# Kernel optimization log

Hardware: AMD Instinct MI355X
Metric: run time of the kernel (lower is better)

## Reference

```python
import jax, jax.numpy as jnp
import numpy as np

P = 30000    # pathway graph nodes
E = 480000   # edges
G = 20000    # genes
MP = 32      # max pathways per gene (padded)
R = 28       # pathway root count
B = 4096     # batch of gene pairs
IN, H, OUT = 394, 256, 64
GD = 128     # params.gene_dim


def setup_inputs() -> dict:
    key = jax.random.key(0)
    ks = iter(jax.random.split(key, 48))
    nx = lambda shape, s=1.0: jax.random.normal(next(ks), shape, dtype=jnp.float32) * s
    inp = {}
    inp["x1"] = nx((P, IN))
    inp["x2"] = nx((P, IN))
    inp["edge_src"] = jax.random.randint(next(ks), (E,), 0, P)
    inp["edge_dst"] = jax.random.randint(next(ks), (E,), 0, P)
    inp["edge_weight"] = jax.random.uniform(next(ks), (E,), dtype=jnp.float32)
    for g in ("g1", "g2"):
        inp[g + "_w1"] = nx((IN, H), 0.05); inp[g + "_b1"] = jnp.zeros((H,), jnp.float32)
        inp[g + "_w2"] = nx((H, OUT), 0.05); inp[g + "_b2"] = jnp.zeros((OUT,), jnp.float32)
    inp["pl1_w"] = nx((OUT * R, 256), 0.02); inp["pl1_b"] = jnp.zeros((256,), jnp.float32)
    inp["bn1_g"] = jnp.ones((256,), jnp.float32); inp["bn1_b"] = jnp.zeros((256,), jnp.float32)
    inp["pl2_w"] = nx((256, GD), 0.05); inp["pl2_b"] = jnp.zeros((GD,), jnp.float32)
    inp["bn2_g"] = jnp.ones((GD,), jnp.float32); inp["bn2_b"] = jnp.zeros((GD,), jnp.float32)
    inp["fc_w"] = nx((2 * GD, 256), 0.05); inp["fc_b"] = jnp.zeros((256,), jnp.float32)
    inp["fc1_w"] = nx((256, 128), 0.05); inp["fc1_b"] = jnp.zeros((128,), jnp.float32)
    inp["fc2_w"] = nx((128, 1), 0.05); inp["fc2_b"] = jnp.zeros((1,), jnp.float32)
    inp["pathway_root"] = jax.random.randint(next(ks), (P,), 0, R)
    inp["gene_paths"] = jax.random.randint(next(ks), (G, MP), 0, P)
    inp["gene_paths_mask"] = jax.random.uniform(next(ks), (G, MP)) < 0.7
    inp["head_ids"] = jax.random.randint(next(ks), (B,), 0, G)
    inp["tail_ids"] = jax.random.randint(next(ks), (B,), 0, G)
    return inp


def gcn_conv(x, w, b, src, dst, ew):
    # PyG GCNConv with edge weights + self loops (fill_value=1), symmetric norm.
    h = x @ w
    deg = jnp.zeros((x.shape[0],), x.dtype).at[dst].add(ew) + 1.0
    norm = jax.lax.rsqrt(deg)
    msg = h[src] * (ew * norm[src] * norm[dst])[:, None]
    agg = jnp.zeros_like(h).at[dst].add(msg) + h * (norm * norm)[:, None]
    return agg + b


def pathway_gcn(x, w1, b1, w2, b2, src, dst, ew):
    h = jax.nn.relu(gcn_conv(x, w1, b1, src, dst, ew))  # F.dropout in eval = identity
    return gcn_conv(h, w2, b2, src, dst, ew)


def gene_pathway_feat(s, gene_ids, gene_paths, gene_paths_mask, pathway_root):
    # Vectorized form of the per-gene python-loop gather + per-root sum.
    paths = gene_paths[gene_ids]                      # [B, MP]
    m = gene_paths_mask[gene_ids].astype(s.dtype)     # [B, MP]
    gathered = s[paths]                               # [B, MP, 64]
    oh = jax.nn.one_hot(pathway_root[paths], R, dtype=s.dtype) * m[..., None]
    feat = jnp.einsum('bpr,bpd->brd', oh, gathered)   # segment-sum into roots
    return feat.reshape(paths.shape[0], R * s.shape[1])


def batchnorm(x, g, b, eps=1e-5):
    mu = x.mean(0)
    var = x.var(0)  # biased, as torch BN training
    return g * (x - mu) * jax.lax.rsqrt(var + eps) + b


def reference(x1, x2, edge_src, edge_dst, edge_weight,
              g1_w1, g1_b1, g1_w2, g1_b2, g2_w1, g2_b1, g2_w2, g2_b2,
              pl1_w, pl1_b, bn1_g, bn1_b, pl2_w, pl2_b, bn2_g, bn2_b,
              fc_w, fc_b, fc1_w, fc1_b, fc2_w, fc2_b,
              pathway_root, gene_paths, gene_paths_mask, head_ids, tail_ids):
    out1 = pathway_gcn(x1, g1_w1, g1_b1, g1_w2, g1_b2, edge_src, edge_dst, edge_weight)
    out2 = pathway_gcn(x2, g2_w1, g2_b1, g2_w2, g2_b2, edge_src, edge_dst, edge_weight)
    s = out1 + out2  # original stacks feats from both graphs per pathway, then sums

    def fuse(ids):
        f = gene_pathway_feat(s, ids, gene_paths, gene_paths_mask, pathway_root)
        h = jax.nn.relu(batchnorm(f @ pl1_w + pl1_b, bn1_g, bn1_b))
        return batchnorm(h @ pl2_w + pl2_b, bn2_g, bn2_b)

    fuse_feat = jnp.concatenate([fuse(head_ids), fuse(tail_ids)], axis=1)  # [B, 2*GD]
    final = jax.nn.relu(fuse_feat @ fc_w + fc_b) @ fc1_w + fc1_b
    return jax.nn.relu(final) @ fc2_w + fc2_b  # [B, 1]
```

## Files before the change

kernel.cpp:

```cpp
#include <hip/hip_runtime.h>
#include <cstdint>

typedef __attribute__((ext_vector_type(4))) float f32x4;
typedef __attribute__((ext_vector_type(8))) short s16x8;

__device__ inline unsigned short f2bf(float f) {
    unsigned u = __float_as_uint(f);
    unsigned r = (u + 0x7FFFu + ((u >> 16) & 1u)) >> 16;
    return (unsigned short)r;
}
__device__ inline float b2f(unsigned short h) {
    return __uint_as_float(((unsigned)h) << 16);
}

__device__ inline void gload16(const unsigned short* g, unsigned short* l) {
    __builtin_amdgcn_global_load_lds(
        (const __attribute__((address_space(1))) unsigned int*)g,
        (__attribute__((address_space(3))) unsigned int*)l, 16, 0, 0);
}

struct TD { const float* in; unsigned short* out; int K, N, Kp, ldo; };

__global__ void prep_kernel(const unsigned char* __restrict__ mask, int maskBytes,
                            int* __restrict__ flag, float* __restrict__ zspan, long long zwords,
                            TD d0, TD d1, TD d2, TD d3, TD d4, TD d5, TD d6, TD d7) {
    int y = blockIdx.y;
    if (y == 0) {
        if (blockIdx.x != 0) return;
        __shared__ int isByte, isFloat;
        if (threadIdx.x == 0) { isByte = 0; isFloat = 0; }
        __syncthreads();
        const unsigned* w = (const unsigned*)mask;
        for (int i = threadIdx.x; i < maskBytes / 4; i += blockDim.x) {
            unsigned v = w[i];
            if (v == 0u || v == 1u) continue;
            if (v == 0x3f800000u) isFloat = 1; else isByte = 1;
        }
        __syncthreads();
        if (threadIdx.x == 0) *flag = isFloat ? 2 : (isByte ? 1 : 0);
        return;
    }
    if (y == 1) {
        long long i = (long long)blockIdx.x * 256 + threadIdx.x;
        if (i < zwords) zspan[i] = 0.f;
        return;
    }
    TD d = d0;
    if (y == 3) d = d1; else if (y == 4) d = d2; else if (y == 5) d = d3;
    else if (y == 6) d = d4; else if (y == 7) d = d5; else if (y == 8) d = d6; else if (y == 9) d = d7;
    int idx = blockIdx.x * 256 + threadIdx.x;
    if (idx >= d.N * d.Kp) return;
    int n = idx / d.Kp, k = idx - n * d.Kp;
    d.out[(size_t)n * d.ldo + k] = (k < d.K) ? f2bf(d.in[(size_t)k * d.N + n]) : (unsigned short)0;
}

__global__ void deg_cnt_kernel(const int* __restrict__ dst, const float* __restrict__ ew,
                               float* __restrict__ degw, int* __restrict__ cnt, int E) {
    int e = blockIdx.x * 256 + threadIdx.x;
    if (e >= E) return;
    int d = dst[e];
    unsafeAtomicAdd(&degw[d], ew[e]);
    atomicAdd(&cnt[d], 1);
}

__global__ __launch_bounds__(1024) void norm_scan_kernel(const int* __restrict__ cnt,
                                                         int* __restrict__ rowstart,
                                                         float* __restrict__ degw, int P) {
    int t = threadIdx.x;
    if (blockIdx.x > 0) {
        int i = (blockIdx.x - 1) * 1024 + t;
        if (i < P) degw[i] = rsqrtf(degw[i] + 1.0f);
        return;
    }
    const int seg = (P + 1023) >> 10;
    int base = t * seg;
    int sum = 0;
    for (int j = 0; j < seg; ++j) {
        int i = base + j;
        if (i < P) sum += cnt[i];
    }
    int lane = t & 63, w = t >> 6;
    int x = sum;
#pragma unroll
    for (int off = 1; off < 64; off <<= 1) {
        int y = __shfl_up(x, off);
        if (lane >= off) x += y;
    }
    __shared__ int wsum[16];
    if (lane == 63) wsum[w] = x;
    __syncthreads();
    int woff = 0;
    for (int i = 0; i < w; ++i) woff += wsum[i];
    int run = woff + x - sum;
    for (int j = 0; j < seg; ++j) {
        int i = base + j;
        if (i < P) { run += cnt[i]; rowstart[i + 1] = run; }
    }
    if (t == 0) rowstart[0] = 0;
}

__global__ void fill_kernel(const int* __restrict__ src, const int* __restrict__ dst,
                            const float* __restrict__ ew, const float* __restrict__ norm,
                            const int* __restrict__ rowstart, int* __restrict__ fill,
                            int* __restrict__ csrc, float* __restrict__ coef, int E) {
    int e = blockIdx.x * 256 + threadIdx.x;
    if (e >= E) return;
    int d = dst[e], sI = src[e];
    int pos = rowstart[d] + atomicAdd(&fill[d], 1);
    csrc[pos] = sI;
    coef[pos] = ew[e] * norm[sI] * norm[d];
}

__global__ __launch_bounds__(256) void conv1_agg_kernel(
    const unsigned short* __restrict__ Hb, const float* __restrict__ norm,
    const int* __restrict__ rowstart, const int* __restrict__ csrc, const float* __restrict__ coef,
    const float* __restrict__ b0, const float* __restrict__ b1,
    unsigned short* __restrict__ out, int P) {
    int node = blockIdx.x * 4 + (threadIdx.x >> 6);
    if (node >= P) return;
    int z = blockIdx.y;
    const unsigned short* H = Hb + (size_t)z * P * 256;
    const float* bias = z ? b1 : b0;
    int lane = threadIdx.x & 63;
    int f4 = lane * 4;
    float nn = norm[node];
    ushort4 hv = *(const ushort4*)(H + (size_t)node * 256 + f4);
    float a0 = b2f(hv.x) * nn * nn, a1 = b2f(hv.y) * nn * nn;
    float a2 = b2f(hv.z) * nn * nn, a3 = b2f(hv.w) * nn * nn;
    int s0 = rowstart[node], s1 = rowstart[node + 1];
    int p = s0;
    for (; p + 4 <= s1; p += 4) {
        int i0 = csrc[p], i1 = csrc[p + 1], i2 = csrc[p + 2], i3 = csrc[p + 3];
        float c0 = coef[p], c1 = coef[p + 1], c2 = coef[p + 2], c3 = coef[p + 3];
        ushort4 v0 = *(const ushort4*)(H + (size_t)i0 * 256 + f4);
        ushort4 v1 = *(const ushort4*)(H + (size_t)i1 * 256 + f4);
        ushort4 v2 = *(const ushort4*)(H + (size_t)i2 * 256 + f4);
        ushort4 v3 = *(const ushort4*)(H + (size_t)i3 * 256 + f4);
        a0 += b2f(v0.x) * c0 + b2f(v1.x) * c1 + b2f(v2.x) * c2 + b2f(v3.x) * c3;
        a1 += b2f(v0.y) * c0 + b2f(v1.y) * c1 + b2f(v2.y) * c2 + b2f(v3.y) * c3;
        a2 += b2f(v0.z) * c0 + b2f(v1.z) * c1 + b2f(v2.z) * c2 + b2f(v3.z) * c3;
        a3 += b2f(v0.w) * c0 + b2f(v1.w) * c1 + b2f(v2.w) * c2 + b2f(v3.w) * c3;
    }
    for (; p < s1; ++p) {
        int i0 = csrc[p];
        float c0 = coef[p];
        ushort4 v0 = *(const ushort4*)(H + (size_t)i0 * 256 + f4);
        a0 += b2f(v0.x) * c0; a1 += b2f(v0.y) * c0; a2 += b2f(v0.z) * c0; a3 += b2f(v0.w) * c0;
    }
    float4 bv = *(const float4*)(bias + f4);
    ushort4 o;
    o.x = f2bf(fmaxf(a0 + bv.x, 0.f));
    o.y = f2bf(fmaxf(a1 + bv.y, 0.f));
    o.z = f2bf(fmaxf(a2 + bv.z, 0.f));
    o.w = f2bf(fmaxf(a3 + bv.w, 0.f));
    *(ushort4*)(out + (size_t)node * 512 + z * 256 + f4) = o;
}

__global__ __launch_bounds__(256) void conv2_agg_kernel(
    const unsigned short* __restrict__ T, const float* __restrict__ norm,
    const int* __restrict__ rowstart, const int* __restrict__ csrc, const float* __restrict__ coef,
    const float* __restrict__ b0, const float* __restrict__ b1,
    float* __restrict__ s, int P) {
    int node = blockIdx.x * 4 + (threadIdx.x >> 6);
    if (node >= P) return;
    int lane = threadIdx.x & 63;
    float nn = norm[node];
    float acc = b2f(T[(size_t)node * 64 + lane]) * nn * nn;
    int s0 = rowstart[node], s1 = rowstart[node + 1];
    int p = s0;
    for (; p + 4 <= s1; p += 4) {
        int i0 = csrc[p], i1 = csrc[p + 1], i2 = csrc[p + 2], i3 = csrc[p + 3];
        float c0 = coef[p], c1 = coef[p + 1], c2 = coef[p + 2], c3 = coef[p + 3];
        acc += b2f(T[(size_t)i0 * 64 + lane]) * c0 + b2f(T[(size_t)i1 * 64 + lane]) * c1 +
               b2f(T[(size_t)i2 * 64 + lane]) * c2 + b2f(T[(size_t)i3 * 64 + lane]) * c3;
    }
    for (; p < s1; ++p) acc += b2f(T[(size_t)csrc[p] * 64 + lane]) * coef[p];
    s[(size_t)node * 64 + lane] = acc + b0[lane] + b1[lane];
}

struct G2 {
    const void* A[2]; const unsigned short* Bt[2]; const float* bias[2];
    float* Cf[2]; unsigned short* Cb[2];
};

template<int BM, int BN, int WM, int WN>
__global__ __launch_bounds__(256) void gemm1_hybrid_kernel(
    const float* __restrict__ x0, const float* __restrict__ x1,
    const unsigned short* __restrict__ Bt0, const unsigned short* __restrict__ Bt1,
    unsigned short* __restrict__ C0, unsigned short* __restrict__ C1,
    int M, int IN, int Kp, int ldc) {
    const int z = blockIdx.z;
    const float* A = z ? x1 : x0;
    const unsigned short* Bt = z ? Bt1 : Bt0;
    unsigned short* Cb = z ? C1 : C0;

    constexpr int LDK = 40;
    __shared__ __align__(16) unsigned short As[2][BM * LDK];
    __shared__ __align__(16) unsigned short Bs[2][BN * 32];
    const int t = threadIdx.x, lane = t & 63, wid = t >> 6;
    constexpr int NWC = BN / WN;
    const int wr = wid / NWC, wc = wid % NWC;
    constexpr int MR = WM / 16, NR = WN / 16;
    static_assert((BM / WM) * (BN / WN) == 4, "4 waves");
    constexpr int BI = BN / 64;
    const int row0 = blockIdx.y * BM, col0 = blockIdx.x * BN;
    const int sr = lane >> 2;
    const int sc = ((lane & 3) ^ ((lane >> 3) & 3)) * 8;
    int brow[BI];
#pragma unroll
    for (int i = 0; i < BI; ++i) brow[i] = col0 + (wid * BI + i) * 16 + sr;
    const int ar = t >> 2, akc = (t & 3) * 8;
    int arowg = row0 + ar; if (arowg >= M) arowg = M - 1;
    const float* aptr = A + (size_t)arowg * IN;

    f32x4 acc[MR][NR] = {};
    const int r16 = lane & 15, q = lane >> 4;
    const int kbA = q * 8;
    const int kbB = ((q ^ ((r16 >> 1) & 3)) * 8);

    auto stageB = [&](int buf, int kt) {
#pragma unroll
        for (int i = 0; i < BI; ++i)
            gload16(Bt + (size_t)brow[i] * Kp + kt + sc, &Bs[buf][(wid * BI + i) * 512]);
    };
    auto loadA = [&](int kt, float* v) {
        int kg = kt + akc;
        if (kg + 8 <= IN) {
            float2 a = *(const float2*)(aptr + kg);
            float2 b = *(const float2*)(aptr + kg + 2);
            float2 c = *(const float2*)(aptr + kg + 4);
            float2 d = *(const float2*)(aptr + kg + 6);
            v[0]=a.x; v[1]=a.y; v[2]=b.x; v[3]=b.y; v[4]=c.x; v[5]=c.y; v[6]=d.x; v[7]=d.y;
        } else {
#pragma unroll
            for (int j = 0; j < 8; ++j) v[j] = (kg + j < IN) ? aptr[kg + j] : 0.f;
        }
    };
    auto writeA = [&](int buf, const float* v) {
        s16x8 w;
#pragma unroll
        for (int j = 0; j < 8; ++j) w[j] = (short)f2bf(v[j]);
        *(s16x8*)&As[buf][ar * LDK + akc] = w;
    };

    {
        float v[8];
        stageB(0, 0);
        loadA(0, v);
        writeA(0, v);
    }
    int cur = 0;
    for (int kt = 0; kt < Kp; kt += 32) {
        __syncthreads();
        float nv[8];
        const bool has = (kt + 32 < Kp);
        if (has) { stageB(cur ^ 1, kt + 32); loadA(kt + 32, nv); }
        s16x8 af[MR], bfr[NR];
#pragma unroll
        for (int m = 0; m < MR; ++m)
            af[m] = *(const s16x8*)&As[cur][(wr * WM + m * 16 + r16) * LDK + kbA];
#pragma unroll
        for (int n = 0; n < NR; ++n)
            bfr[n] = *(const s16x8*)&Bs[cur][(wc * WN + n * 16 + r16) * 32 + kbB];
#pragma unroll
        for (int m = 0; m < MR; ++m)
#pragma unroll
            for (int n = 0; n < NR; ++n)
                acc[m][n] = __builtin_amdgcn_mfma_f32_16x16x32_bf16(af[m], bfr[n], acc[m][n], 0, 0, 0);
        if (has) writeA(cur ^ 1, nv);
        cur ^= 1;
    }
#pragma unroll
    for (int m = 0; m < MR; ++m)
#pragma unroll
        for (int n = 0; n < NR; ++n) {
            int col = col0 + wc * WN + n * 16 + r16;
#pragma unroll
            for (int r = 0; r < 4; ++r) {
                int row = row0 + wr * WM + m * 16 + q * 4 + r;
                if (row < M) Cb[(size_t)row * ldc + col] = f2bf(acc[m][n][r]);
            }
        }
}

template<int BM, int BN, int WM, int WN>
__global__ __launch_bounds__(256) void m97s_gemm_kernel(
    G2 g, int M, int Kp, int lda, int ldc, int relu) {
    const int z = blockIdx.z;
    const unsigned short* A = (const unsigned short*)(z ? g.A[1] : g.A[0]);
    const unsigned short* Bt = z ? g.Bt[1] : g.Bt[0];
    const float* bias = z ? g.bias[1] : g.bias[0];
    float* Cf = z ? g.Cf[1] : g.Cf[0];
    unsigned short* Cb = z ? g.Cb[1] : g.Cb[0];

    __shared__ __align__(16) unsigned short As[2][BM * 32];
    __shared__ __align__(16) unsigned short Bs[2][BN * 32];
    const int t = threadIdx.x, lane = t & 63, wid = t >> 6;
    constexpr int NWC = BN / WN;
    const int wr = wid / NWC, wc = wid % NWC;
    constexpr int MR = WM / 16, NR = WN / 16;
    static_assert((BM / WM) * (BN / WN) == 4, "4 waves");
    constexpr int AI = BM / 64, BI = BN / 64;
    const int row0 = blockIdx.y * BM, col0 = blockIdx.x * BN;
    const int sr = lane >> 2;
    const int sc = ((lane & 3) ^ ((lane >> 3) & 3)) * 8;
    int arow[AI];
#pragma unroll
    for (int i = 0; i < AI; ++i) {
        int r = row0 + (wid * AI + i) * 16 + sr;
        arow[i] = r < M ? r : M - 1;
    }
    int brow[BI];
#pragma unroll
    for (int i = 0; i < BI; ++i) brow[i] = col0 + (wid * BI + i) * 16 + sr;

    f32x4 acc[MR][NR] = {};
    const int r16 = lane & 15;
    const int kb = (((lane >> 4) ^ ((r16 >> 1) & 3)) * 8);

    auto stage = [&](int buf, int kt) {
#pragma unroll
        for (int i = 0; i < AI; ++i)
            gload16(A + (size_t)arow[i] * lda + kt + sc, &As[buf][(wid * AI + i) * 512]);
#pragma unroll
        for (int i = 0; i < BI; ++i)
            gload16(Bt + (size_t)brow[i] * Kp + kt + sc, &Bs[buf][(wid * BI + i) * 512]);
    };

    stage(0, 0);
    int cur = 0;
    for (int kt = 0; kt < Kp; kt += 32) {
        __syncthreads();
        if (kt + 32 < Kp) stage(cur ^ 1, kt + 32);
        s16x8 af[MR], bfr[NR];
#pragma unroll
        for (int m = 0; m < MR; ++m)
            af[m] = *(const s16x8*)&As[cur][(wr * WM + m * 16 + r16) * 32 + kb];
#pragma unroll
        for (int n = 0; n < NR; ++n)
            bfr[n] = *(const s16x8*)&Bs[cur][(wc * WN + n * 16 + r16) * 32 + kb];
#pragma unroll
        for (int m = 0; m < MR; ++m)
#pragma unroll
            for (int n = 0; n < NR; ++n)
                acc[m][n] = __builtin_amdgcn_mfma_f32_16x16x32_bf16(af[m], bfr[n], acc[m][n], 0, 0, 0);
        cur ^= 1;
    }
#pragma unroll
    for (int m = 0; m < MR; ++m)
#pragma unroll
        for (int n = 0; n < NR; ++n) {
            int col = col0 + wc * WN + n * 16 + r16;
#pragma unroll
            for (int r = 0; r < 4; ++r) {
                int row = row0 + wr * WM + m * 16 + (lane >> 4) * 4 + r;
                if (row < M) {
                    float v = acc[m][n][r] + (bias ? bias[col] : 0.f);
                    if (relu) v = fmaxf(v, 0.f);
                    if (Cf) Cf[(size_t)row * ldc + col] = v;
                    if (Cb) Cb[(size_t)row * ldc + col] = f2bf(v);
                }
            }
        }
}

template<int BM, int BN, int WM, int WN>
__global__ __launch_bounds__(256) void pl1_stats_kernel(
    G2 g, int M, int Kp, int lda, int ldc, float* __restrict__ statsPart, int C) {
    const int z = blockIdx.z;
    const unsigned short* A = (const unsigned short*)(z ? g.A[1] : g.A[0]);
    const unsigned short* Bt = z ? g.Bt[1] : g.Bt[0];
    const float* bias = z ? g.bias[1] : g.bias[0];
    float* Cf = z ? g.Cf[1] : g.Cf[0];

    __shared__ __align__(16) unsigned short As[2][BM * 32];
    __shared__ __align__(16) unsigned short Bs[2][BN * 32];
    const int t = threadIdx.x, lane = t & 63, wid = t >> 6;
    constexpr int NWC = BN / WN;
    const int wr = wid / NWC, wc = wid % NWC;
    constexpr int MR = WM / 16, NR = WN / 16;
    constexpr int AI = BM / 64, BI = BN / 64;
    const int row0 = blockIdx.y * BM, col0 = blockIdx.x * BN;
    const int sr = lane >> 2;
    const int sc = ((lane & 3) ^ ((lane >> 3) & 3)) * 8;
    int arow[AI];
#pragma unroll
    for (int i = 0; i < AI; ++i) {
        int r = row0 + (wid * AI + i) * 16 + sr;
        arow[i] = r < M ? r : M - 1;
    }
    int brow[BI];
#pragma unroll
    for (int i = 0; i < BI; ++i) brow[i] = col0 + (wid * BI + i) * 16 + sr;

    f32x4 acc[MR][NR] = {};
    const int r16 = lane & 15, q = lane >> 4;
    const int kb = ((q ^ ((r16 >> 1) & 3)) * 8);

    auto stage = [&](int buf, int kt) {
#pragma unroll
        for (int i = 0; i < AI; ++i)
            gload16(A + (size_t)arow[i] * lda + kt + sc, &As[buf][(wid * AI + i) * 512]);
#pragma unroll
        for (int i = 0; i < BI; ++i)
            gload16(Bt + (size_t)brow[i] * Kp + kt + sc, &Bs[buf][(wid * BI + i) * 512]);
    };

    stage(0, 0);
    int cur = 0;
    for (int kt = 0; kt < Kp; kt += 32) {
        __syncthreads();
        if (kt + 32 < Kp) stage(cur ^ 1, kt + 32);
        s16x8 af[MR], bfr[NR];
#pragma unroll
        for (int m = 0; m < MR; ++m)
            af[m] = *(const s16x8*)&As[cur][(wr * WM + m * 16 + r16) * 32 + kb];
#pragma unroll
        for (int n = 0; n < NR; ++n)
            bfr[n] = *(const s16x8*)&Bs[cur][(wc * WN + n * 16 + r16) * 32 + kb];
#pragma unroll
        for (int m = 0; m < MR; ++m)
#pragma unroll
            for (int n = 0; n < NR; ++n)
                acc[m][n] = __builtin_amdgcn_mfma_f32_16x16x32_bf16(af[m], bfr[n], acc[m][n], 0, 0, 0);
        cur ^= 1;
    }
    float* sp = statsPart + (size_t)z * 2 * C;
#pragma unroll
    for (int n = 0; n < NR; ++n) {
        int col = col0 + wc * WN + n * 16 + r16;
        float sm = 0.f, sq = 0.f;
#pragma unroll
        for (int m = 0; m < MR; ++m)
#pragma unroll
            for (int r = 0; r < 4; ++r) {
                int row = row0 + wr * WM + m * 16 + q * 4 + r;
                float v = acc[m][n][r] + bias[col];
                Cf[(size_t)row * ldc + col] = v;
                sm += v; sq += v * v;
            }
        sm += __shfl_xor(sm, 16); sq += __shfl_xor(sq, 16);
        sm += __shfl_xor(sm, 32); sq += __shfl_xor(sq, 32);
        if (lane < 16) {
            unsafeAtomicAdd(&sp[col], sm);
            unsafeAtomicAdd(&sp[C + col], sq);
        }
    }
}

template<int BM, int BN, int WM, int WN>
__global__ __launch_bounds__(256) void pl2_bn_stats_kernel(
    const float* __restrict__ z1, const unsigned short* __restrict__ Bt,
    const float* __restrict__ bias, float* __restrict__ z2,
    const float* __restrict__ bn1part, const float* __restrict__ bn1g, const float* __restrict__ bn1b,
    float* __restrict__ bn2part, int Mrows, int Kp, int ldc) {
    const int z = blockIdx.z;
    const float* A = z1 + (size_t)z * Mrows * Kp;
    float* Cf = z2 + (size_t)z * Mrows * ldc;

    constexpr int LDK = 40;
    __shared__ __align__(16) unsigned short As[BM * LDK];
    __shared__ __align__(16) unsigned short Bs[BN * 32];
    __shared__ float sc1[256], sh1[256];
    const int t = threadIdx.x, lane = t & 63, wid = t >> 6;
    {
        const float* bp = bn1part + (size_t)z * 2 * 256;
        float mu = bp[t] / Mrows;
        float var = bp[256 + t] / Mrows - mu * mu;
        float rstd = rsqrtf(var + 1e-5f);
        float s = rstd * bn1g[t];
        sc1[t] = s; sh1[t] = bn1b[t] - mu * s;
    }
    constexpr int NWC = BN / WN;
    const int wr = wid / NWC, wc = wid % NWC;
    constexpr int MR = WM / 16, NR = WN / 16;
    constexpr int BI = BN / 64;
    const int row0 = blockIdx.y * BM, col0 = blockIdx.x * BN;
    const int sr = lane >> 2;
    const int sc = ((lane & 3) ^ ((lane >> 3) & 3)) * 8;
    int brow[BI];
#pragma unroll
    for (int i = 0; i < BI; ++i) brow[i] = col0 + (wid * BI + i) * 16 + sr;
    const int ar = t >> 2, akc = (t & 3) * 8;
    const float* aptr = A + (size_t)(row0 + ar) * Kp;
    f32x4 acc[MR][NR] = {};
    const int r16 = lane & 15, q = lane >> 4;
    const int kbA = q * 8;
    const int kbB = ((q ^ ((r16 >> 1) & 3)) * 8);
    __syncthreads();

    for (int kt = 0; kt < Kp; kt += 32) {
#pragma unroll
        for (int i = 0; i < BI; ++i)
            gload16(Bt + (size_t)brow[i] * Kp + kt + sc, &Bs[(wid * BI + i) * 512]);
        {
            int kg = kt + akc;
            float4 a = *(const float4*)(aptr + kg);
            float4 b = *(const float4*)(aptr + kg + 4);
            float v[8] = {a.x, a.y, a.z, a.w, b.x, b.y, b.z, b.w};
            s16x8 w;
#pragma unroll
            for (int j = 0; j < 8; ++j)
                w[j] = (short)f2bf(fmaxf(v[j] * sc1[kg + j] + sh1[kg + j], 0.f));
            *(s16x8*)&As[ar * LDK + akc] = w;
        }
        __syncthreads();
        s16x8 af[MR], bfr[NR];
#pragma unroll
        for (int m = 0; m < MR; ++m)
            af[m] = *(const s16x8*)&As[(wr * WM + m * 16 + r16) * LDK + kbA];
#pragma unroll
        for (int n = 0; n < NR; ++n)
            bfr[n] = *(const s16x8*)&Bs[(wc * WN + n * 16 + r16) * 32 + kbB];
#pragma unroll
        for (int m = 0; m < MR; ++m)
#pragma unroll
            for (int n = 0; n < NR; ++n)
                acc[m][n] = __builtin_amdgcn_mfma_f32_16x16x32_bf16(af[m], bfr[n], acc[m][n], 0, 0, 0);
        __syncthreads();
    }
    float* sp = bn2part + (size_t)z * 2 * ldc;
#pragma unroll
    for (int n = 0; n < NR; ++n) {
        int col = col0 + wc * WN + n * 16 + r16;
        float sm = 0.f, sq = 0.f;
#pragma unroll
        for (int m = 0; m < MR; ++m)
#pragma unroll
            for (int r = 0; r < 4; ++r) {
                int row = row0 + wr * WM + m * 16 + q * 4 + r;
                float v = acc[m][n][r] + bias[col];
                Cf[(size_t)row * ldc + col] = v;
                sm += v; sq += v * v;
            }
        sm += __shfl_xor(sm, 16); sq += __shfl_xor(sq, 16);
        sm += __shfl_xor(sm, 32); sq += __shfl_xor(sq, 32);
        if (lane < 16) {
            unsafeAtomicAdd(&sp[col], sm);
            unsafeAtomicAdd(&sp[ldc + col], sq);
        }
    }
}

__global__ __launch_bounds__(64) void gene_feat_kernel(
    const float* __restrict__ S, const int* __restrict__ head, const int* __restrict__ tail,
    const int* __restrict__ gene_paths, const void* __restrict__ mask,
    const int* __restrict__ root, unsigned short* __restrict__ feat, const int* __restrict__ flag,
    int B) {
    __shared__ float lds[28 * 64];
    int lane = threadIdx.x;
#pragma unroll
    for (int i = 0; i < 28; ++i) lds[i * 64 + lane] = 0.f;
    int side = blockIdx.y;
    const int* ids = side ? tail : head;
    int gene = ids[blockIdx.x];
    int fl = *flag;
    const unsigned char* mb = (const unsigned char*)mask;
    const int* mi = (const int*)mask;
    const float* mf = (const float*)mask;
    for (int p = 0; p < 32; ++p) {
        int idx = gene * 32 + p;
        int m = (fl == 0) ? mi[idx] : (fl == 1) ? (int)mb[idx] : (mf[idx] != 0.f);
        if (!m) continue;
        int path = gene_paths[idx];
        int r = root[path];
        lds[r * 64 + lane] += S[(size_t)path * 64 + lane];
    }
    unsigned short* frow = feat + ((size_t)side * B + blockIdx.x) * 1792;
#pragma unroll
    for (int i = 0; i < 28; ++i) frow[i * 64 + lane] = f2bf(lds[i * 64 + lane]);
}

__global__ __launch_bounds__(256) void mlp_tail_kernel(
    const float* __restrict__ z2, const float* __restrict__ bn2part,
    const float* __restrict__ bn2g, const float* __restrict__ bn2b,
    const unsigned short* __restrict__ fct, const float* __restrict__ fc_b,
    const unsigned short* __restrict__ fc1t, const float* __restrict__ fc1_b,
    const float* __restrict__ fc2_w, const float* __restrict__ fc2_b,
    float* __restrict__ out, int B) {
    constexpr int LDK = 40;
    __shared__ __align__(16) unsigned short As[64 * LDK];
    __shared__ __align__(16) unsigned short Bs[256 * 32];
    __shared__ __align__(16) unsigned short T1[64 * 264];
    __shared__ float part[64];
    __shared__ float sc2[256], sh2[256];
    const int t = threadIdx.x, lane = t & 63, wid = t >> 6;
    const int row0 = blockIdx.x * 64;
    const int sr = lane >> 2, sc = ((lane & 3) ^ ((lane >> 3) & 3)) * 8;
    const int r16 = lane & 15, q = lane >> 4;
    const int kbA = q * 8;
    const int kbB = ((q ^ ((r16 >> 1) & 3)) * 8);
    const int ar = t >> 2, akc = (t & 3) * 8;

    {
        int side = t >> 7, cc = t & 127;
        const float* bp = bn2part + (size_t)side * 256;
        float mu = bp[cc] / B;
        float var = bp[128 + cc] / B - mu * mu;
        float rstd = rsqrtf(var + 1e-5f);
        float s = rstd * bn2g[cc];
        sc2[t] = s; sh2[t] = bn2b[cc] - mu * s;
    }
    __syncthreads();

    {
        f32x4 acc[4][4] = {};
        int brow[4];
#pragma unroll
        for (int i = 0; i < 4; ++i) brow[i] = (wid * 4 + i) * 16 + sr;
        for (int kt = 0; kt < 256; kt += 32) {
#pragma unroll
            for (int i = 0; i < 4; ++i)
                gload16(fct + (size_t)brow[i] * 256 + kt + sc, &Bs[(wid * 4 + i) * 512]);
            {
                int c0 = kt + akc;
                int side = c0 >> 7, cc = c0 & 127;
                const float* zr = z2 + ((size_t)side * B + row0 + ar) * 128 + cc;
                float4 a = *(const float4*)zr;
                float4 b = *(const float4*)(zr + 4);
                float v[8] = {a.x, a.y, a.z, a.w, b.x, b.y, b.z, b.w};
                s16x8 w;
#pragma unroll
                for (int j = 0; j < 8; ++j) w[j] = (short)f2bf(v[j] * sc2[c0 + j] + sh2[c0 + j]);
                *(s16x8*)&As[ar * LDK + akc] = w;
            }
            __syncthreads();
            s16x8 af[4], bfr[4];
#pragma unroll
            for (int m = 0; m < 4; ++m) af[m] = *(const s16x8*)&As[(m * 16 + r16) * LDK + kbA];
#pragma unroll
            for (int n = 0; n < 4; ++n) bfr[n] = *(const s16x8*)&Bs[(wid * 64 + n * 16 + r16) * 32 + kbB];
#pragma unroll
            for (int m = 0; m < 4; ++m)
#pragma unroll
                for (int n = 0; n < 4; ++n)
                    acc[m][n] = __builtin_amdgcn_mfma_f32_16x16x32_bf16(af[m], bfr[n], acc[m][n], 0, 0, 0);
            __syncthreads();
        }
#pragma unroll
        for (int m = 0; m < 4; ++m)
#pragma unroll
            for (int n = 0; n < 4; ++n) {
                int col = wid * 64 + n * 16 + r16;
#pragma unroll
                for (int r = 0; r < 4; ++r) {
                    int row = m * 16 + q * 4 + r;
                    T1[row * 264 + col] = f2bf(fmaxf(acc[m][n][r] + fc_b[col], 0.f));
                }
            }
    }
    __syncthreads();
    if (t < 64) part[t] = 0.f;

    f32x4 acc2[4][2] = {};
    {
        int brow[2];
#pragma unroll
        for (int i = 0; i < 2; ++i) brow[i] = (wid * 2 + i) * 16 + sr;
        for (int kt = 0; kt < 256; kt += 32) {
#pragma unroll
            for (int i = 0; i < 2; ++i)
                gload16(fc1t + (size_t)brow[i] * 256 + kt + sc, &Bs[(wid * 2 + i) * 512]);
            __syncthreads();
            s16x8 af[4], bfr[2];
#pragma unroll
            for (int m = 0; m < 4; ++m) af[m] = *(const s16x8*)&T1[(m * 16 + r16) * 264 + kt + q * 8];
#pragma unroll
            for (int n = 0; n < 2; ++n) bfr[n] = *(const s16x8*)&Bs[(wid * 32 + n * 16 + r16) * 32 + kbB];
#pragma unroll
            for (int m = 0; m < 4; ++m)
#pragma unroll
                for (int n = 0; n < 2; ++n)
                    acc2[m][n] = __builtin_amdgcn_mfma_f32_16x16x32_bf16(af[m], bfr[n], acc2[m][n], 0, 0, 0);
            __syncthreads();
        }
    }
#pragma unroll
    for (int m = 0; m < 4; ++m)
#pragma unroll
        for (int r = 0; r < 4; ++r) {
            float sv = 0.f;
#pragma unroll
            for (int n = 0; n < 2; ++n) {
                int col = wid * 32 + n * 16 + r16;
                float v = fmaxf(acc2[m][n][r] + fc1_b[col], 0.f);
                sv += v * fc2_w[col];
            }
#pragma unroll
            for (int off = 1; off < 16; off <<= 1) sv += __shfl_xor(sv, off);
            if (r16 == 0) atomicAdd(&part[m * 16 + q * 4 + r], sv);
        }
    __syncthreads();
    if (t < 64 && row0 + t < B) out[row0 + t] = part[t] + fc2_b[0];
}

extern "C" void kernel_launch(void* const* d_in, const int* in_sizes, int n_in,
                              void* d_out, int out_size, void* d_ws, size_t ws_size,
                              hipStream_t stream) {
    const float* x[2] = {(const float*)d_in[0], (const float*)d_in[1]};
    const int* esrc = (const int*)d_in[2];
    const int* edst = (const int*)d_in[3];
    const float* ew = (const float*)d_in[4];
    const float* g_w1[2] = {(const float*)d_in[5], (const float*)d_in[9]};
    const float* g_b1[2] = {(const float*)d_in[6], (const float*)d_in[10]};
    const float* g_w2[2] = {(const float*)d_in[7], (const float*)d_in[11]};
    const float* g_b2[2] = {(const float*)d_in[8], (const float*)d_in[12]};
    const float* pl1_w = (const float*)d_in[13];
    const float* pl1_b = (const float*)d_in[14];
    const float* bn1_g = (const float*)d_in[15];
    const float* bn1_b = (const float*)d_in[16];
    const float* pl2_w = (const float*)d_in[17];
    const float* pl2_b = (const float*)d_in[18];
    const float* bn2_g = (const float*)d_in[19];
    const float* bn2_b = (const float*)d_in[20];
    const float* fc_w = (const float*)d_in[21];
    const float* fc_b = (const float*)d_in[22];
    const float* fc1_w = (const float*)d_in[23];
    const float* fc1_b = (const float*)d_in[24];
    const float* fc2_w = (const float*)d_in[25];
    const float* fc2_b = (const float*)d_in[26];
    const int* root = (const int*)d_in[27];
    const int* gene_paths = (const int*)d_in[28];
    const void* gmask = d_in[29];
    const int* head = (const int*)d_in[30];
    const int* tail = (const int*)d_in[31];

    const int P = in_sizes[27];
    const int E = in_sizes[2];
    const int B = in_sizes[30];
    const int IN = 394, Kp1 = 416, H = 256, OUT = 64, GD = 128;
    const int MB = (P + 63) / 64;

    char* ws = (char*)d_ws;
    size_t off = 0;
    auto alloc = [&](size_t bytes) -> char* {
        char* p = ws + off;
        off = (off + bytes + 255) & ~(size_t)255;
        return p;
    };
    int* flag = (int*)alloc(256);
    float* norm = (float*)alloc((size_t)P * 4);
    int* cnt = (int*)alloc((size_t)P * 4);
    int* fillp = (int*)alloc((size_t)P * 4);
    float* bn1part = (float*)alloc((size_t)2 * 2 * 256 * 4);
    float* bn2part = (float*)alloc((size_t)2 * 2 * 128 * 4);
    char* zend = ws + off;
    int* rowstart = (int*)alloc((size_t)(P + 1) * 4);
    int* csrc = (int*)alloc((size_t)E * 4);
    float* coef = (float*)alloc((size_t)E * 4);
    unsigned short* W1t = (unsigned short*)alloc((size_t)2 * H * Kp1 * 2);
    unsigned short* W2tc = (unsigned short*)alloc((size_t)OUT * 512 * 2);
    unsigned short* pl1t = (unsigned short*)alloc((size_t)256 * 1792 * 2);
    unsigned short* pl2t = (unsigned short*)alloc((size_t)GD * 256 * 2);
    unsigned short* fct = (unsigned short*)alloc((size_t)256 * 256 * 2);
    unsigned short* fc1t = (unsigned short*)alloc((size_t)GD * 256 * 2);
    unsigned short* bufH = (unsigned short*)alloc((size_t)2 * P * H * 2);
    unsigned short* bufh1 = (unsigned short*)alloc((size_t)P * 512 * 2);
    float* s = (float*)alloc((size_t)P * OUT * 4);
    (void)n_in; (void)out_size; (void)ws_size;

    unsigned short* bufh2 = bufH;
    unsigned short* feat = bufh1;
    char* mlp = (char*)bufH + 4194304;
    size_t mo = 0;
    auto malloc2 = [&](size_t bytes) -> char* {
        char* p = mlp + mo;
        mo = (mo + bytes + 255) & ~(size_t)255;
        return p;
    };
    float* z1 = (float*)malloc2((size_t)2 * B * 256 * 4);
    float* z2 = (float*)malloc2((size_t)2 * B * GD * 4);

    {
        long long zwords = (zend - (char*)norm) / 4;
        TD d0 = {g_w1[0], W1t, IN, H, Kp1, Kp1};
        TD d1 = {g_w1[1], W1t + (size_t)H * Kp1, IN, H, Kp1, Kp1};
        TD d2 = {g_w2[0], W2tc, H, OUT, H, 512};
        TD d3 = {g_w2[1], W2tc + 256, H, OUT, H, 512};
        TD d4 = {pl1_w, pl1t, 1792, 256, 1792, 1792};
        TD d5 = {pl2_w, pl2t, 256, GD, 256, 256};
        TD d6 = {fc_w, fct, 256, 256, 256, 256};
        TD d7 = {fc1_w, fc1t, 256, GD, 256, 256};
        prep_kernel<<<dim3(1792, 10), 256, 0, stream>>>(
            (const unsigned char*)gmask, 4096, flag, norm, zwords,
            d0, d1, d2, d3, d4, d5, d6, d7);
    }

    deg_cnt_kernel<<<(E + 255) / 256, 256, 0, stream>>>(edst, ew, norm, cnt, E);
    norm_scan_kernel<<<1 + (P + 1023) / 1024, 1024, 0, stream>>>(cnt, rowstart, norm, P);
    fill_kernel<<<(E + 255) / 256, 256, 0, stream>>>(esrc, edst, ew, norm, rowstart, fillp, csrc, coef, E);

    gemm1_hybrid_kernel<64, 128, 32, 64><<<dim3(H / 128, MB, 2), 256, 0, stream>>>(
        x[0], x[1], W1t, W1t + (size_t)H * Kp1, bufH, bufH + (size_t)P * H, P, IN, Kp1, H);

    conv1_agg_kernel<<<dim3((P + 3) / 4, 2), 256, 0, stream>>>(bufH, norm, rowstart, csrc, coef,
                                                               g_b1[0], g_b1[1], bufh1, P);
    {
        G2 g = {{bufh1, nullptr}, {W2tc, nullptr}, {nullptr, nullptr},
                {nullptr, nullptr}, {bufh2, nullptr}};
        m97s_gemm_kernel<64, 64, 32, 32><<<dim3(1, MB, 1), 256, 0, stream>>>(
            g, P, 512, 512, OUT, 0);
    }
    conv2_agg_kernel<<<dim3((P + 3) / 4), 256, 0, stream>>>(bufh2, norm, rowstart, csrc, coef,
                                                            g_b2[0], g_b2[1], s, P);

    gene_feat_kernel<<<dim3(B, 2), 64, 0, stream>>>(s, head, tail, gene_paths, gmask, root, feat, flag, B);

    {
        G2 g = {{feat, feat + (size_t)B * 1792}, {pl1t, pl1t}, {pl1_b, pl1_b},
                {z1, z1 + (size_t)B * 256}, {nullptr, nullptr}};
        pl1_stats_kernel<64, 128, 32, 64><<<dim3(2, B / 64, 2), 256, 0, stream>>>(
            g, B, 1792, 1792, 256, bn1part, 256);
    }
    pl2_bn_stats_kernel<64, 64, 32, 32><<<dim3(2, B / 64, 2), 256, 0, stream>>>(
        z1, pl2t, pl2_b, z2, bn1part, bn1_g, bn1_b, bn2part, B, 256, GD);

    mlp_tail_kernel<<<B / 64, 256, 0, stream>>>(z2, bn2part, bn2_g, bn2_b, fct, fc_b,
                                                fc1t, fc1_b, fc2_w, fc2_b, (float*)d_out, B);
}
```

Measured before the change: 369.8 us.

## Retile first GCN GEMM to full-width 32-row blocks and unroll aggregation by eight

The first-layer GEMM now gives each block 32 rows and the full 256-column output width, with four waves split across N. Each fp32 row of x is therefore read and converted to bf16 once instead of once per column tile, and the A-staging thread mapping changes to four elements per thread. The conv1 aggregation gathers eight neighbours per iteration to raise memory-level parallelism. The pl1 GEMM switches to 64x64 tiles with more blocks. Together these trade more register pressure and B-tile traffic for less redundant A loading and better latency hiding.

```diff
diff --git a/kernel.cpp b/kernel.cpp
--- a/kernel.cpp
+++ b/kernel.cpp
@@ -129,6 +129,28 @@
     float a2 = b2f(hv.z) * nn * nn, a3 = b2f(hv.w) * nn * nn;
     int s0 = rowstart[node], s1 = rowstart[node + 1];
     int p = s0;
+    for (; p + 8 <= s1; p += 8) {
+        int i0 = csrc[p], i1 = csrc[p + 1], i2 = csrc[p + 2], i3 = csrc[p + 3];
+        int i4 = csrc[p + 4], i5 = csrc[p + 5], i6 = csrc[p + 6], i7 = csrc[p + 7];
+        float c0 = coef[p], c1 = coef[p + 1], c2 = coef[p + 2], c3 = coef[p + 3];
+        float c4 = coef[p + 4], c5 = coef[p + 5], c6 = coef[p + 6], c7 = coef[p + 7];
+        ushort4 v0 = *(const ushort4*)(H + (size_t)i0 * 256 + f4);
+        ushort4 v1 = *(const ushort4*)(H + (size_t)i1 * 256 + f4);
+        ushort4 v2 = *(const ushort4*)(H + (size_t)i2 * 256 + f4);
+        ushort4 v3 = *(const ushort4*)(H + (size_t)i3 * 256 + f4);
+        ushort4 v4 = *(const ushort4*)(H + (size_t)i4 * 256 + f4);
+        ushort4 v5 = *(const ushort4*)(H + (size_t)i5 * 256 + f4);
+        ushort4 v6 = *(const ushort4*)(H + (size_t)i6 * 256 + f4);
+        ushort4 v7 = *(const ushort4*)(H + (size_t)i7 * 256 + f4);
+        a0 += b2f(v0.x) * c0 + b2f(v1.x) * c1 + b2f(v2.x) * c2 + b2f(v3.x) * c3
+            + b2f(v4.x) * c4 + b2f(v5.x) * c5 + b2f(v6.x) * c6 + b2f(v7.x) * c7;
+        a1 += b2f(v0.y) * c0 + b2f(v1.y) * c1 + b2f(v2.y) * c2 + b2f(v3.y) * c3
+            + b2f(v4.y) * c4 + b2f(v5.y) * c5 + b2f(v6.y) * c6 + b2f(v7.y) * c7;
+        a2 += b2f(v0.z) * c0 + b2f(v1.z) * c1 + b2f(v2.z) * c2 + b2f(v3.z) * c3
+            + b2f(v4.z) * c4 + b2f(v5.z) * c5 + b2f(v6.z) * c6 + b2f(v7.z) * c7;
+        a3 += b2f(v0.w) * c0 + b2f(v1.w) * c1 + b2f(v2.w) * c2 + b2f(v3.w) * c3
+            + b2f(v4.w) * c4 + b2f(v5.w) * c5 + b2f(v6.w) * c6 + b2f(v7.w) * c7;
+    }
     for (; p + 4 <= s1; p += 4) {
         int i0 = csrc[p], i1 = csrc[p + 1], i2 = csrc[p + 2], i3 = csrc[p + 3];
         float c0 = coef[p], c1 = coef[p + 1], c2 = coef[p + 2], c3 = coef[p + 3];
@@ -183,7 +205,7 @@
     float* Cf[2]; unsigned short* Cb[2];
 };
 
-template<int BM, int BN, int WM, int WN>
+template<int BN, int WN>
 __global__ __launch_bounds__(256) void gemm1_hybrid_kernel(
     const float* __restrict__ x0, const float* __restrict__ x1,
     const unsigned short* __restrict__ Bt0, const unsigned short* __restrict__ Bt1,
@@ -194,22 +216,21 @@
     const unsigned short* Bt = z ? Bt1 : Bt0;
     unsigned short* Cb = z ? C1 : C0;
 
-    constexpr int LDK = 40;
+    constexpr int BM = 32, LDK = 40;
     __shared__ __align__(16) unsigned short As[2][BM * LDK];
     __shared__ __align__(16) unsigned short Bs[2][BN * 32];
     const int t = threadIdx.x, lane = t & 63, wid = t >> 6;
-    constexpr int NWC = BN / WN;
-    const int wr = wid / NWC, wc = wid % NWC;
-    constexpr int MR = WM / 16, NR = WN / 16;
-    static_assert((BM / WM) * (BN / WN) == 4, "4 waves");
+    constexpr int MR = 2, NR = WN / 16;
+    static_assert(BN / WN == 4, "4 waves in N");
     constexpr int BI = BN / 64;
     const int row0 = blockIdx.y * BM, col0 = blockIdx.x * BN;
+    const int wc = wid;
     const int sr = lane >> 2;
     const int sc = ((lane & 3) ^ ((lane >> 3) & 3)) * 8;
     int brow[BI];
 #pragma unroll
     for (int i = 0; i < BI; ++i) brow[i] = col0 + (wid * BI + i) * 16 + sr;
-    const int ar = t >> 2, akc = (t & 3) * 8;
+    const int ar = t >> 3, akc = (t & 7) * 4;
     int arowg = row0 + ar; if (arowg >= M) arowg = M - 1;
     const float* aptr = A + (size_t)arowg * IN;
 
@@ -225,26 +246,23 @@
     };
     auto loadA = [&](int kt, float* v) {
         int kg = kt + akc;
-        if (kg + 8 <= IN) {
+        if (kg + 4 <= IN) {
             float2 a = *(const float2*)(aptr + kg);
             float2 b = *(const float2*)(aptr + kg + 2);
-            float2 c = *(const float2*)(aptr + kg + 4);
-            float2 d = *(const float2*)(aptr + kg + 6);
-            v[0]=a.x; v[1]=a.y; v[2]=b.x; v[3]=b.y; v[4]=c.x; v[5]=c.y; v[6]=d.x; v[7]=d.y;
+            v[0] = a.x; v[1] = a.y; v[2] = b.x; v[3] = b.y;
         } else {
 #pragma unroll
-            for (int j = 0; j < 8; ++j) v[j] = (kg + j < IN) ? aptr[kg + j] : 0.f;
+            for (int j = 0; j < 4; ++j) v[j] = (kg + j < IN) ? aptr[kg + j] : 0.f;
         }
     };
     auto writeA = [&](int buf, const float* v) {
-        s16x8 w;
-#pragma unroll
-        for (int j = 0; j < 8; ++j) w[j] = (short)f2bf(v[j]);
-        *(s16x8*)&As[buf][ar * LDK + akc] = w;
+        ushort4 w;
+        w.x = f2bf(v[0]); w.y = f2bf(v[1]); w.z = f2bf(v[2]); w.w = f2bf(v[3]);
+        *(ushort4*)&As[buf][ar * LDK + akc] = w;
     };
 
     {
-        float v[8];
+        float v[4];
         stageB(0, 0);
         loadA(0, v);
         writeA(0, v);
@@ -252,13 +270,13 @@
     int cur = 0;
     for (int kt = 0; kt < Kp; kt += 32) {
         __syncthreads();
-        float nv[8];
+        float nv[4];
         const bool has = (kt + 32 < Kp);
         if (has) { stageB(cur ^ 1, kt + 32); loadA(kt + 32, nv); }
         s16x8 af[MR], bfr[NR];
 #pragma unroll
         for (int m = 0; m < MR; ++m)
-            af[m] = *(const s16x8*)&As[cur][(wr * WM + m * 16 + r16) * LDK + kbA];
+            af[m] = *(const s16x8*)&As[cur][(m * 16 + r16) * LDK + kbA];
 #pragma unroll
         for (int n = 0; n < NR; ++n)
             bfr[n] = *(const s16x8*)&Bs[cur][(wc * WN + n * 16 + r16) * 32 + kbB];
@@ -277,7 +295,7 @@
             int col = col0 + wc * WN + n * 16 + r16;
 #pragma unroll
             for (int r = 0; r < 4; ++r) {
-                int row = row0 + wr * WM + m * 16 + q * 4 + r;
+                int row = row0 + m * 16 + q * 4 + r;
                 if (row < M) Cb[(size_t)row * ldc + col] = f2bf(acc[m][n][r]);
             }
         }
@@ -730,6 +748,7 @@
     const int B = in_sizes[30];
     const int IN = 394, Kp1 = 416, H = 256, OUT = 64, GD = 128;
     const int MB = (P + 63) / 64;
+    const int MB32 = (P + 31) / 32;
 
     char* ws = (char*)d_ws;
     size_t off = 0;
@@ -790,7 +809,7 @@
     norm_scan_kernel<<<1 + (P + 1023) / 1024, 1024, 0, stream>>>(cnt, rowstart, norm, P);
     fill_kernel<<<(E + 255) / 256, 256, 0, stream>>>(esrc, edst, ew, norm, rowstart, fillp, csrc, coef, E);
 
-    gemm1_hybrid_kernel<64, 128, 32, 64><<<dim3(H / 128, MB, 2), 256, 0, stream>>>(
+    gemm1_hybrid_kernel<256, 64><<<dim3(1, MB32, 2), 256, 0, stream>>>(
         x[0], x[1], W1t, W1t + (size_t)H * Kp1, bufH, bufH + (size_t)P * H, P, IN, Kp1, H);
 
     conv1_agg_kernel<<<dim3((P + 3) / 4, 2), 256, 0, stream>>>(bufH, norm, rowstart, csrc, coef,
@@ -809,7 +828,7 @@
     {
         G2 g = {{feat, feat + (size_t)B * 1792}, {pl1t, pl1t}, {pl1_b, pl1_b},
                 {z1, z1 + (size_t)B * 256}, {nullptr, nullptr}};
-        pl1_stats_kernel<64, 128, 32, 64><<<dim3(2, B / 64, 2), 256, 0, stream>>>(
+        pl1_stats_kernel<64, 64, 32, 32><<<dim3(4, B / 64, 2), 256, 0, stream>>>(
             g, B, 1792, 1792, 256, bn1part, 256);
     }
     pl2_bn_stats_kernel<64, 64, 32, 32><<<dim3(2, B / 64, 2), 256, 0, stream>>>(
```

New measurement: 364.5 us. No clear change (-1.4%).
